# Kernel optimization log

Measured on AMD Instinct MI355X. Metric: run time of the kernel, lower is better.

## Reference

```python
import jax, jax.numpy as jnp
import numpy as np

N = 50000
TOPK = 32
IN_C = 128
OUT_C = 64
NEG_SLOPE = 0.2
BN_EPS = 1e-5


def setup_inputs() -> dict:
    key = jax.random.key(0)
    ks = jax.random.split(key, 8)
    x = jax.random.normal(ks[0], (N, IN_C), dtype=jnp.float32)
    embedding = jax.random.normal(ks[1], (N, OUT_C), dtype=jnp.float32)
    # edges: each node has TOPK incoming edges, no self loops
    tgt = jnp.repeat(jnp.arange(N, dtype=jnp.int64), TOPK)
    off = jax.random.randint(ks[2], (N * TOPK,), 1, N, dtype=jnp.int64)
    src = (tgt + off) % N
    edge_index = jnp.stack([src, tgt], axis=0)
    lin_w = jax.random.normal(ks[3], (OUT_C, IN_C), dtype=jnp.float32) * (1.0 / np.sqrt(IN_C))
    att_i = jax.random.normal(ks[4], (1, 1, OUT_C), dtype=jnp.float32) * 0.1
    att_j = jax.random.normal(ks[5], (1, 1, OUT_C), dtype=jnp.float32) * 0.1
    att_em_i = jax.random.normal(ks[6], (1, 1, OUT_C), dtype=jnp.float32) * 0.1
    att_em_j = jax.random.normal(ks[7], (1, 1, OUT_C), dtype=jnp.float32) * 0.1
    bias = jnp.zeros((OUT_C,), dtype=jnp.float32)
    bn_gamma = jnp.ones((OUT_C,), dtype=jnp.float32)
    bn_beta = jnp.zeros((OUT_C,), dtype=jnp.float32)
    return {"x": x, "embedding": embedding, "edge_index": edge_index,
            "lin_w": lin_w, "att_i": att_i, "att_j": att_j,
            "att_em_i": att_em_i, "att_em_j": att_em_j, "bias": bias,
            "bn_gamma": bn_gamma, "bn_beta": bn_beta}


def _gnn_forward(x, embedding, lin_w, att_i, att_j, att_em_i, att_em_j,
                 bias, bn_gamma, bn_beta, src, tgt):
    n = x.shape[0]
    # linear transform: [N, heads=1, OUT_C]
    x_lin = (x @ lin_w.T).reshape(n, 1, OUT_C)
    # gather per edge (self loops already appended to src/tgt)
    x_i = x_lin[tgt]                      # [Etot, 1, C]
    x_j = x_lin[src]                      # [Etot, 1, C]
    emb_i = embedding[tgt][:, None, :]    # [Etot, 1, C]
    emb_j = embedding[src][:, None, :]
    # attention logits, eq (6)-(8)
    alpha = ((x_i * att_i).sum(-1) + (emb_i * att_em_i).sum(-1)
             + (x_j * att_j).sum(-1) + (emb_j * att_em_j).sum(-1))  # [Etot, 1]
    alpha = jnp.where(alpha >= 0, alpha, NEG_SLOPE * alpha)
    # segment softmax over incoming edges of each target node
    m = jax.ops.segment_max(alpha, tgt, num_segments=n)
    m = jnp.where(jnp.isfinite(m), m, 0.0)
    e = jnp.exp(alpha - m[tgt])
    denom = jax.ops.segment_sum(e, tgt, num_segments=n)
    alpha = e / (denom[tgt] + 1e-16)      # [Etot, 1]
    # weighted scatter-add aggregation
    msg = x_j * alpha[:, :, None]         # [Etot, 1, C]
    out = jax.ops.segment_sum(msg, tgt, num_segments=n).reshape(n, OUT_C)
    out = out + bias
    # BatchNorm1d (training-mode batch stats, biased var) + ReLU
    mu = out.mean(axis=0)
    var = ((out - mu) ** 2).mean(axis=0)
    out = (out - mu) / jnp.sqrt(var + BN_EPS) * bn_gamma + bn_beta
    return jax.nn.relu(out)


def reference(x, embedding, edge_index, lin_w, att_i, att_j, att_em_i,
              att_em_j, bias, bn_gamma, bn_beta):
    n = x.shape[0]
    loops = jnp.arange(n, dtype=edge_index.dtype)
    src = jnp.concatenate([edge_index[0], loops])
    tgt = jnp.concatenate([edge_index[1], loops])
    return _gnn_forward(x, embedding, lin_w, att_i, att_j, att_em_i,
                        att_em_j, bias, bn_gamma, bn_beta, src, tgt)
```

## Files before the change

kernel.cpp:

```cpp
#include <hip/hip_runtime.h>

#define NN 50000
#define TOPK 32
#define IN_C 128
#define OUT_C 64
#define NEG_SLOPE 0.2f
#define BN_EPS 1e-5f

#define K1_BLOCKS (NN / 16)
#define K2_BLOCKS (NN / 8)

#define WS_XBF   0
#define WS_AI    (NN * 32)
#define WS_AJ    (WS_AI + NN)
#define WS_SUMS  (WS_AJ + NN)

typedef __bf16 bf16x8 __attribute__((ext_vector_type(8)));
typedef float f32x4 __attribute__((ext_vector_type(4)));
union BF8 { unsigned short u[8]; bf16x8 v; };

__device__ inline float leaky(float a) { return a >= 0.f ? a : NEG_SLOPE * a; }
__device__ inline float bl(unsigned u) { return __uint_as_float(u << 16); }
__device__ inline float bh(unsigned u) { return __uint_as_float(u & 0xffff0000u); }

__device__ inline unsigned short f2bf(float f) {
    unsigned u = __float_as_uint(f);
    unsigned r = (u + 0x7fffu + ((u >> 16) & 1u)) >> 16;
    return (unsigned short)r;
}

__device__ inline void async16(const uint4* g, uint4* l) {
    __builtin_amdgcn_global_load_lds(
        (const __attribute__((address_space(1))) void*)(const void*)g,
        (__attribute__((address_space(3))) void*)(void*)l, 16, 0, 0);
}

__global__ __launch_bounds__(256) void k1_mfma(
    const float* __restrict__ x, const float* __restrict__ emb,
    const float* __restrict__ lin_w,
    const float* __restrict__ att_i, const float* __restrict__ att_j,
    const float* __restrict__ att_em_i, const float* __restrict__ att_em_j,
    unsigned short* __restrict__ x_bf, float* __restrict__ a_i,
    float* __restrict__ a_j, float* __restrict__ sums)
{
    __shared__ float redi[16][5], redj[16][5];
    __shared__ float eredi[16][17], eredj[16][17];
    const int tid = threadIdx.x;
    if (blockIdx.x == 0) {
#pragma unroll
        for (int i = 0; i < 4; ++i) sums[tid + i * 256] = 0.f;
    }

    const int lane = tid & 63;
    const int wv = tid >> 6;
    const int quad = lane >> 4;
    const int nn = lane & 15;
    const int base = blockIdx.x * 16;
    const int c = wv * 16 + nn;

    BF8 bfr[4], afr[4];
    {
        const float* wr = lin_w + (size_t)c * IN_C + quad * 8;
        const float* xr = x + (size_t)(base + nn) * IN_C + quad * 8;
#pragma unroll
        for (int s = 0; s < 4; ++s) {
            const float4 wa = *(const float4*)(wr + s * 32);
            const float4 wb = *(const float4*)(wr + s * 32 + 4);
            const float4 xa = *(const float4*)(xr + s * 32);
            const float4 xb = *(const float4*)(xr + s * 32 + 4);
            bfr[s].u[0] = f2bf(wa.x); bfr[s].u[1] = f2bf(wa.y);
            bfr[s].u[2] = f2bf(wa.z); bfr[s].u[3] = f2bf(wa.w);
            bfr[s].u[4] = f2bf(wb.x); bfr[s].u[5] = f2bf(wb.y);
            bfr[s].u[6] = f2bf(wb.z); bfr[s].u[7] = f2bf(wb.w);
            afr[s].u[0] = f2bf(xa.x); afr[s].u[1] = f2bf(xa.y);
            afr[s].u[2] = f2bf(xa.z); afr[s].u[3] = f2bf(xa.w);
            afr[s].u[4] = f2bf(xb.x); afr[s].u[5] = f2bf(xb.y);
            afr[s].u[6] = f2bf(xb.z); afr[s].u[7] = f2bf(xb.w);
        }
    }

    f32x4 acc = {0.f, 0.f, 0.f, 0.f};
#pragma unroll
    for (int s = 0; s < 4; ++s)
        acc = __builtin_amdgcn_mfma_f32_16x16x32_bf16(afr[s].v, bfr[s].v, acc,
                                                      0, 0, 0);

    const float aic = att_i[c], ajc = att_j[c];
    float pi[4], pj[4];
#pragma unroll
    for (int r = 0; r < 4; ++r) {
        const int node = base + quad * 4 + r;
        x_bf[(size_t)node * OUT_C + c] = f2bf(acc[r]);
        pi[r] = acc[r] * aic;
        pj[r] = acc[r] * ajc;
    }
#pragma unroll
    for (int d = 1; d < 16; d <<= 1) {
#pragma unroll
        for (int r = 0; r < 4; ++r) {
            pi[r] += __shfl_xor(pi[r], d, 64);
            pj[r] += __shfl_xor(pj[r], d, 64);
        }
    }
    if (nn == 0) {
#pragma unroll
        for (int r = 0; r < 4; ++r) {
            redi[quad * 4 + r][wv] = pi[r];
            redj[quad * 4 + r][wv] = pj[r];
        }
    }
    {
        const int nl = tid >> 4, c4 = tid & 15;
        const float4 e4 = ((const float4*)emb)[(size_t)(base + nl) * 16 + c4];
        const float4 i4 = ((const float4*)att_em_i)[c4];
        const float4 j4 = ((const float4*)att_em_j)[c4];
        eredi[nl][c4] = e4.x * i4.x + e4.y * i4.y + e4.z * i4.z + e4.w * i4.w;
        eredj[nl][c4] = e4.x * j4.x + e4.y * j4.y + e4.z * j4.z + e4.w * j4.w;
    }
    __syncthreads();
    if (tid < 16) {
        float si = redi[tid][0] + redi[tid][1] + redi[tid][2] + redi[tid][3];
        float sj = redj[tid][0] + redj[tid][1] + redj[tid][2] + redj[tid][3];
#pragma unroll
        for (int r = 0; r < 16; ++r) { si += eredi[tid][r]; sj += eredj[tid][r]; }
        a_i[base + tid] = si;
        a_j[base + tid] = sj;
    }
}

__global__ __launch_bounds__(64) void k2_attn(
    const int* __restrict__ src, const uint4* __restrict__ x_bf4,
    const float* __restrict__ a_j, const float* __restrict__ a_i,
    const float* __restrict__ bias, float* __restrict__ out,
    float* __restrict__ sums)
{
    __shared__ uint4 stage[33 * 64];
    __shared__ float wbuf[8][36];
    __shared__ float sb1[64][9], sb2[64][9];

    const int tid = threadIdx.x;
    const int g = tid >> 3;
    const int q = tid & 7;
    const int t = blockIdx.x * 8 + g;

    const int4* sp4 = (const int4*)(src + (size_t)t * TOPK);
    int4 s4[8];
#pragma unroll
    for (int i = 0; i < 8; ++i) s4[i] = sp4[i];
    const int4 sq = sp4[q];

#pragma unroll
    for (int i = 0; i < 8; ++i) {
        async16(x_bf4 + ((size_t)s4[i].x * 8 + q), &stage[(i * 4 + 0) * 64]);
        async16(x_bf4 + ((size_t)s4[i].y * 8 + q), &stage[(i * 4 + 1) * 64]);
        async16(x_bf4 + ((size_t)s4[i].z * 8 + q), &stage[(i * 4 + 2) * 64]);
        async16(x_bf4 + ((size_t)s4[i].w * 8 + q), &stage[(i * 4 + 3) * 64]);
    }
    async16(x_bf4 + ((size_t)t * 8 + q), &stage[32 * 64]);

    const float ai_t = a_i[t];
    float l0 = leaky(ai_t + a_j[sq.x]);
    float l1 = leaky(ai_t + a_j[sq.y]);
    float l2 = leaky(ai_t + a_j[sq.z]);
    float l3 = leaky(ai_t + a_j[sq.w]);
    const float ls = leaky(ai_t + a_j[t]);
    float mx = fmaxf(fmaxf(l0, l1), fmaxf(l2, l3));
#pragma unroll
    for (int d = 1; d < 8; d <<= 1) mx = fmaxf(mx, __shfl_xor(mx, d, 64));
    mx = fmaxf(mx, ls);
    const float e0 = __expf(l0 - mx), e1 = __expf(l1 - mx);
    const float e2 = __expf(l2 - mx), e3 = __expf(l3 - mx);
    const float es = __expf(ls - mx);
    float den = (e0 + e1) + (e2 + e3);
#pragma unroll
    for (int d = 1; d < 8; d <<= 1) den += __shfl_xor(den, d, 64);
    den += es + 1e-16f;
    const float inv = 1.f / den;

    ((float4*)&wbuf[g][q * 4])[0] =
        make_float4(e0 * inv, e1 * inv, e2 * inv, e3 * inv);
    if (q == 0) wbuf[g][32] = es * inv;
    __syncthreads();

    float4 w4[8];
#pragma unroll
    for (int i = 0; i < 8; ++i) w4[i] = ((const float4*)wbuf[g])[i];
    const float wself = wbuf[g][32];

    __builtin_amdgcn_s_waitcnt(0x0F70);
    __syncthreads();

    float A[8];
#pragma unroll
    for (int j = 0; j < 8; ++j) A[j] = 0.f;
#pragma unroll
    for (int e = 0; e < 33; ++e) {
        const uint4 u = stage[e * 64 + tid];
        const float w = (e < 32) ? ((const float*)&w4[e >> 2])[e & 3] : wself;
        A[0] = fmaf(w, bl(u.x), A[0]); A[1] = fmaf(w, bh(u.x), A[1]);
        A[2] = fmaf(w, bl(u.y), A[2]); A[3] = fmaf(w, bh(u.y), A[3]);
        A[4] = fmaf(w, bl(u.z), A[4]); A[5] = fmaf(w, bh(u.z), A[5]);
        A[6] = fmaf(w, bl(u.w), A[6]); A[7] = fmaf(w, bh(u.w), A[7]);
    }
    const float4 b0 = ((const float4*)bias)[q * 2];
    const float4 b1 = ((const float4*)bias)[q * 2 + 1];
    float v[8];
    v[0] = A[0] + b0.x; v[1] = A[1] + b0.y; v[2] = A[2] + b0.z; v[3] = A[3] + b0.w;
    v[4] = A[4] + b1.x; v[5] = A[5] + b1.y; v[6] = A[6] + b1.z; v[7] = A[7] + b1.w;
    float4* o4 = (float4*)(out + (size_t)t * OUT_C + q * 8);
    o4[0] = make_float4(v[0], v[1], v[2], v[3]);
    o4[1] = make_float4(v[4], v[5], v[6], v[7]);

#pragma unroll
    for (int j = 0; j < 8; ++j) {
        sb1[q * 8 + j][g] = v[j];
        sb2[q * 8 + j][g] = v[j] * v[j];
    }
    __syncthreads();
    {
        float t1 = 0.f, t2 = 0.f;
#pragma unroll
        for (int r = 0; r < 8; ++r) { t1 += sb1[tid][r]; t2 += sb2[tid][r]; }
        float* rep = sums + (blockIdx.x & 7) * 128;
        atomicAdd(&rep[tid], t1);
        atomicAdd(&rep[64 + tid], t2);
    }
}

__global__ __launch_bounds__(256) void k4_bn(
    float* __restrict__ out, const float* __restrict__ sums,
    const float* __restrict__ gamma, const float* __restrict__ beta)
{
    __shared__ float s_sc[64], s_sh[64];
    const int tid = threadIdx.x;
    if (tid < 64) {
        float s1 = 0.f, s2 = 0.f;
#pragma unroll
        for (int r = 0; r < 8; ++r) {
            s1 += sums[r * 128 + tid];
            s2 += sums[r * 128 + 64 + tid];
        }
        const float mu = s1 / (float)NN;
        const float ex2 = s2 / (float)NN;
        const float var = fmaxf(ex2 - mu * mu, 0.f);
        const float sc = gamma[tid] / sqrtf(var + BN_EPS);
        s_sc[tid] = sc;
        s_sh[tid] = beta[tid] - mu * sc;
    }
    __syncthreads();
    const int total = NN * OUT_C / 4;
    float4* p = (float4*)out;
    for (int idx = blockIdx.x * 256 + tid; idx < total; idx += gridDim.x * 256) {
        float4 v = p[idx];
        const int c0 = (idx & 15) * 4;
        v.x = fmaxf(fmaf(v.x, s_sc[c0 + 0], s_sh[c0 + 0]), 0.f);
        v.y = fmaxf(fmaf(v.y, s_sc[c0 + 1], s_sh[c0 + 1]), 0.f);
        v.z = fmaxf(fmaf(v.z, s_sc[c0 + 2], s_sh[c0 + 2]), 0.f);
        v.w = fmaxf(fmaf(v.w, s_sc[c0 + 3], s_sh[c0 + 3]), 0.f);
        p[idx] = v;
    }
}

extern "C" void kernel_launch(void* const* d_in, const int* in_sizes, int n_in,
                              void* d_out, int out_size, void* d_ws, size_t ws_size,
                              hipStream_t stream) {
    const float* x        = (const float*)d_in[0];
    const float* emb      = (const float*)d_in[1];
    const int*   edge     = (const int*)d_in[2];
    const float* lin_w    = (const float*)d_in[3];
    const float* att_i    = (const float*)d_in[4];
    const float* att_j    = (const float*)d_in[5];
    const float* att_em_i = (const float*)d_in[6];
    const float* att_em_j = (const float*)d_in[7];
    const float* bias     = (const float*)d_in[8];
    const float* gamma    = (const float*)d_in[9];
    const float* beta     = (const float*)d_in[10];

    float* ws    = (float*)d_ws;
    unsigned short* x_bf = (unsigned short*)(ws + WS_XBF);
    float* a_i   = ws + WS_AI;
    float* a_j   = ws + WS_AJ;
    float* sums  = ws + WS_SUMS;
    float* out   = (float*)d_out;

    k1_mfma<<<K1_BLOCKS, 256, 0, stream>>>(x, emb, lin_w, att_i, att_j,
                                           att_em_i, att_em_j, x_bf, a_i, a_j, sums);
    k2_attn<<<K2_BLOCKS, 64, 0, stream>>>(edge, (const uint4*)x_bf, a_j, a_i,
                                          bias, out, sums);
    k4_bn<<<1024, 256, 0, stream>>>(out, sums, gamma, beta);
}
```

Baseline: 161.7 us.

## Replace LDS-staged gather with register-pipelined shuffled loads in attention kernel

The attention kernel drops the 33-row LDS staging buffer filled by async global-to-LDS loads. It now gathers neighbour rows straight into three rotating register buffers, broadcasting source indices and softmax weights with wave shuffles, so loads overlap with accumulation. The BN partial-sum reduction moves from an LDS transpose to xor-shuffles, which removes every __syncthreads, and launch bounds now request four blocks per CU. The bf16 conversion in k1 switches to native packed casts. The trade-off is more register pressure and shuffle instructions in exchange for zero LDS use and higher occupancy, with less latency hidden per wave than the fully asynchronous prefetch gave.

```diff
diff --git a/kernel.cpp b/kernel.cpp
--- a/kernel.cpp
+++ b/kernel.cpp
@@ -17,22 +17,21 @@
 
 typedef __bf16 bf16x8 __attribute__((ext_vector_type(8)));
 typedef float f32x4 __attribute__((ext_vector_type(4)));
-union BF8 { unsigned short u[8]; bf16x8 v; };
+union BF8 { unsigned p[4]; bf16x8 v; };
 
 __device__ inline float leaky(float a) { return a >= 0.f ? a : NEG_SLOPE * a; }
 __device__ inline float bl(unsigned u) { return __uint_as_float(u << 16); }
 __device__ inline float bh(unsigned u) { return __uint_as_float(u & 0xffff0000u); }
 
+__device__ inline unsigned pk2bf(float lo, float hi) {
+    union { __bf16 b[2]; unsigned u; } cv;
+    cv.b[0] = (__bf16)lo; cv.b[1] = (__bf16)hi;
+    return cv.u;
+}
 __device__ inline unsigned short f2bf(float f) {
-    unsigned u = __float_as_uint(f);
-    unsigned r = (u + 0x7fffu + ((u >> 16) & 1u)) >> 16;
-    return (unsigned short)r;
-}
-
-__device__ inline void async16(const uint4* g, uint4* l) {
-    __builtin_amdgcn_global_load_lds(
-        (const __attribute__((address_space(1))) void*)(const void*)g,
-        (__attribute__((address_space(3))) void*)(void*)l, 16, 0, 0);
+    union { __bf16 b; unsigned short u; } cv;
+    cv.b = (__bf16)f;
+    return cv.u;
 }
 
 __global__ __launch_bounds__(256) void k1_mfma(
@@ -68,14 +67,14 @@
             const float4 wb = *(const float4*)(wr + s * 32 + 4);
             const float4 xa = *(const float4*)(xr + s * 32);
             const float4 xb = *(const float4*)(xr + s * 32 + 4);
-            bfr[s].u[0] = f2bf(wa.x); bfr[s].u[1] = f2bf(wa.y);
-            bfr[s].u[2] = f2bf(wa.z); bfr[s].u[3] = f2bf(wa.w);
-            bfr[s].u[4] = f2bf(wb.x); bfr[s].u[5] = f2bf(wb.y);
-            bfr[s].u[6] = f2bf(wb.z); bfr[s].u[7] = f2bf(wb.w);
-            afr[s].u[0] = f2bf(xa.x); afr[s].u[1] = f2bf(xa.y);
-            afr[s].u[2] = f2bf(xa.z); afr[s].u[3] = f2bf(xa.w);
-            afr[s].u[4] = f2bf(xb.x); afr[s].u[5] = f2bf(xb.y);
-            afr[s].u[6] = f2bf(xb.z); afr[s].u[7] = f2bf(xb.w);
+            bfr[s].p[0] = pk2bf(wa.x, wa.y);
+            bfr[s].p[1] = pk2bf(wa.z, wa.w);
+            bfr[s].p[2] = pk2bf(wb.x, wb.y);
+            bfr[s].p[3] = pk2bf(wb.z, wb.w);
+            afr[s].p[0] = pk2bf(xa.x, xa.y);
+            afr[s].p[1] = pk2bf(xa.z, xa.w);
+            afr[s].p[2] = pk2bf(xb.x, xb.y);
+            afr[s].p[3] = pk2bf(xb.z, xb.w);
         }
     }
 
@@ -128,35 +127,41 @@
     }
 }
 
-__global__ __launch_bounds__(64) void k2_attn(
+__device__ inline void accr(float* A, const uint4 u, const float w) {
+    A[0] = fmaf(w, bl(u.x), A[0]); A[1] = fmaf(w, bh(u.x), A[1]);
+    A[2] = fmaf(w, bl(u.y), A[2]); A[3] = fmaf(w, bh(u.y), A[3]);
+    A[4] = fmaf(w, bl(u.z), A[4]); A[5] = fmaf(w, bh(u.z), A[5]);
+    A[6] = fmaf(w, bl(u.w), A[6]); A[7] = fmaf(w, bh(u.w), A[7]);
+}
+
+__global__ __launch_bounds__(64, 4) void k2_attn(
     const int* __restrict__ src, const uint4* __restrict__ x_bf4,
     const float* __restrict__ a_j, const float* __restrict__ a_i,
     const float* __restrict__ bias, float* __restrict__ out,
     float* __restrict__ sums)
 {
-    __shared__ uint4 stage[33 * 64];
-    __shared__ float wbuf[8][36];
-    __shared__ float sb1[64][9], sb2[64][9];
-
     const int tid = threadIdx.x;
     const int g = tid >> 3;
     const int q = tid & 7;
+    const int gb = tid & 56;
     const int t = blockIdx.x * 8 + g;
 
-    const int4* sp4 = (const int4*)(src + (size_t)t * TOPK);
-    int4 s4[8];
-#pragma unroll
-    for (int i = 0; i < 8; ++i) s4[i] = sp4[i];
-    const int4 sq = sp4[q];
-
-#pragma unroll
-    for (int i = 0; i < 8; ++i) {
-        async16(x_bf4 + ((size_t)s4[i].x * 8 + q), &stage[(i * 4 + 0) * 64]);
-        async16(x_bf4 + ((size_t)s4[i].y * 8 + q), &stage[(i * 4 + 1) * 64]);
-        async16(x_bf4 + ((size_t)s4[i].z * 8 + q), &stage[(i * 4 + 2) * 64]);
-        async16(x_bf4 + ((size_t)s4[i].w * 8 + q), &stage[(i * 4 + 3) * 64]);
-    }
-    async16(x_bf4 + ((size_t)t * 8 + q), &stage[32 * 64]);
+    const int4 sq = ((const int4*)(src + (size_t)t * TOPK))[q];
+    const uint4 rs = x_bf4[(size_t)t * 8 + q];
+
+#define LOADB(dst, b) do {                                                  \
+        const int i0_ = __shfl(sq.x, gb + (b), 64);                         \
+        const int i1_ = __shfl(sq.y, gb + (b), 64);                         \
+        const int i2_ = __shfl(sq.z, gb + (b), 64);                         \
+        const int i3_ = __shfl(sq.w, gb + (b), 64);                         \
+        dst[0] = x_bf4[(size_t)i0_ * 8 + q];                                \
+        dst[1] = x_bf4[(size_t)i1_ * 8 + q];                                \
+        dst[2] = x_bf4[(size_t)i2_ * 8 + q];                                \
+        dst[3] = x_bf4[(size_t)i3_ * 8 + q];                                \
+    } while (0)
+
+    uint4 rA[4], rB[4], rC[4];
+    LOADB(rA, 0); LOADB(rB, 1); LOADB(rC, 2);
 
     const float ai_t = a_i[t];
     float l0 = leaky(ai_t + a_j[sq.x]);
@@ -176,32 +181,32 @@
     for (int d = 1; d < 8; d <<= 1) den += __shfl_xor(den, d, 64);
     den += es + 1e-16f;
     const float inv = 1.f / den;
-
-    ((float4*)&wbuf[g][q * 4])[0] =
-        make_float4(e0 * inv, e1 * inv, e2 * inv, e3 * inv);
-    if (q == 0) wbuf[g][32] = es * inv;
-    __syncthreads();
-
-    float4 w4[8];
-#pragma unroll
-    for (int i = 0; i < 8; ++i) w4[i] = ((const float4*)wbuf[g])[i];
-    const float wself = wbuf[g][32];
-
-    __builtin_amdgcn_s_waitcnt(0x0F70);
-    __syncthreads();
+    const float w0 = e0 * inv, w1 = e1 * inv, w2 = e2 * inv, w3 = e3 * inv;
+    const float wself = es * inv;
 
     float A[8];
 #pragma unroll
     for (int j = 0; j < 8; ++j) A[j] = 0.f;
-#pragma unroll
-    for (int e = 0; e < 33; ++e) {
-        const uint4 u = stage[e * 64 + tid];
-        const float w = (e < 32) ? ((const float*)&w4[e >> 2])[e & 3] : wself;
-        A[0] = fmaf(w, bl(u.x), A[0]); A[1] = fmaf(w, bh(u.x), A[1]);
-        A[2] = fmaf(w, bl(u.y), A[2]); A[3] = fmaf(w, bh(u.y), A[3]);
-        A[4] = fmaf(w, bl(u.z), A[4]); A[5] = fmaf(w, bh(u.z), A[5]);
-        A[6] = fmaf(w, bl(u.w), A[6]); A[7] = fmaf(w, bh(u.w), A[7]);
-    }
+
+#define ACCB(r, b) do {                                                     \
+        const float wx_ = __shfl(w0, gb + (b), 64);                         \
+        const float wy_ = __shfl(w1, gb + (b), 64);                         \
+        const float wz_ = __shfl(w2, gb + (b), 64);                         \
+        const float ww_ = __shfl(w3, gb + (b), 64);                         \
+        accr(A, (r)[0], wx_); accr(A, (r)[1], wy_);                         \
+        accr(A, (r)[2], wz_); accr(A, (r)[3], ww_);                         \
+    } while (0)
+
+    ACCB(rA, 0); LOADB(rA, 3);
+    ACCB(rB, 1); LOADB(rB, 4);
+    ACCB(rC, 2); LOADB(rC, 5);
+    ACCB(rA, 3); LOADB(rA, 6);
+    ACCB(rB, 4); LOADB(rB, 7);
+    ACCB(rC, 5);
+    ACCB(rA, 6);
+    ACCB(rB, 7);
+    accr(A, rs, wself);
+
     const float4 b0 = ((const float4*)bias)[q * 2];
     const float4 b1 = ((const float4*)bias)[q * 2 + 1];
     float v[8];
@@ -211,20 +216,27 @@
     o4[0] = make_float4(v[0], v[1], v[2], v[3]);
     o4[1] = make_float4(v[4], v[5], v[6], v[7]);
 
-#pragma unroll
-    for (int j = 0; j < 8; ++j) {
-        sb1[q * 8 + j][g] = v[j];
-        sb2[q * 8 + j][g] = v[j] * v[j];
-    }
-    __syncthreads();
-    {
-        float t1 = 0.f, t2 = 0.f;
-#pragma unroll
-        for (int r = 0; r < 8; ++r) { t1 += sb1[tid][r]; t2 += sb2[tid][r]; }
+    float s1[8], s2[8];
+#pragma unroll
+    for (int j = 0; j < 8; ++j) { s1[j] = v[j]; s2[j] = v[j] * v[j]; }
+#pragma unroll
+    for (int d = 8; d < 64; d <<= 1) {
+#pragma unroll
+        for (int j = 0; j < 8; ++j) {
+            s1[j] += __shfl_xor(s1[j], d, 64);
+            s2[j] += __shfl_xor(s2[j], d, 64);
+        }
+    }
+    if (tid < 8) {
         float* rep = sums + (blockIdx.x & 7) * 128;
-        atomicAdd(&rep[tid], t1);
-        atomicAdd(&rep[64 + tid], t2);
-    }
+#pragma unroll
+        for (int j = 0; j < 8; ++j) {
+            atomicAdd(&rep[tid * 8 + j], s1[j]);
+            atomicAdd(&rep[64 + tid * 8 + j], s2[j]);
+        }
+    }
+#undef LOADB
+#undef ACCB
 }
 
 __global__ __launch_bounds__(256) void k4_bn(
```

Result: slower. 331.3 us (+104.9%).
